# Kernel tuning notes

Measured on AMD Instinct MI355X. Metric: run time of the kernel, lower is better.

The kernel has to match this reference:

```python
import jax, jax.numpy as jnp
import numpy as np

B, T, H, V = 2, 1024, 4096, 32000
IGNORE_INDEX = -100
BETA = 0.1


def setup_inputs() -> dict:
    key = jax.random.key(0)
    k = jax.random.split(key, 6)
    scale = 1.0 / np.sqrt(H)  # Linear default init scale
    return {
        "x": jax.random.normal(k[0], (B, T, H), jnp.float32),
        "ref_x": jax.random.normal(k[1], (B, T, H), jnp.float32),
        "y": jax.random.randint(k[2], (B, T), 0, V),
        "preference_labels": jax.random.randint(k[3], (B,), 0, 2).astype(bool),
        "W": jax.random.normal(k[4], (V, H), jnp.float32) * scale,
        "ref_W": jax.random.normal(k[5], (V, H), jnp.float32) * scale,
    }


def _avg_logp(h, W, y):
    # h: (B,T,H), W: (V,H), y: (B,T) -> per-sequence average target log-prob (B,)
    logits = jnp.einsum("bth,vh->btv", h, W)
    logp = jax.nn.log_softmax(logits, axis=-1)
    tok_logp = jnp.take_along_axis(logp, jnp.clip(y, 0, V - 1)[..., None], axis=-1)[..., 0]
    mask = (y != IGNORE_INDEX).astype(tok_logp.dtype)
    # average_log_prob=True: mean over non-ignored tokens
    return jnp.sum(tok_logp * mask, axis=-1) / jnp.maximum(jnp.sum(mask, axis=-1), 1.0)


def reference(x, ref_x, y, preference_labels, W, ref_W):
    policy_logps = _avg_logp(x, W, y)            # (B,)
    ref_logps = _avg_logp(ref_x, ref_W, y)       # (B,), no-grad path in original
    logratios = policy_logps - ref_logps
    multiplier = jnp.where(preference_labels, 1.0, -1.0)
    # KTO loss with kl=None: 1 - sigmoid(beta * logratios * multiplier)
    losses = 1.0 - jax.nn.sigmoid(BETA * logratios * multiplier)
    return jnp.sum(losses) / y.shape[0]
```

## Files before the change

### kernel.cpp

```cpp
#include <hip/hip_runtime.h>
#include <hip/hip_bf16.h>
#include <math.h>

#define TT 1024
#define MM 2048
#define HH 4096
#define VV 32000
#define BETA_ 0.1f
#define NPB (VV/64)

#define BM 256
#define BN 256
#define BK 64
#define NT (HH/BK)

typedef short short8 __attribute__((ext_vector_type(8)));
typedef float f32x4 __attribute__((ext_vector_type(4)));

__device__ inline unsigned f2bf1(float f) {
    union { float f; unsigned u; } v; v.f = f;
    return (v.u + 0x7fffu + ((v.u >> 16) & 1u)) >> 16;
}
__device__ inline uint2 pack4(float4 a) {
    uint2 r;
    r.x = f2bf1(a.x) | (f2bf1(a.y) << 16);
    r.y = f2bf1(a.z) | (f2bf1(a.w) << 16);
    return r;
}

__device__ __forceinline__ void gload_lds16(const void* g, void* l) {
    __builtin_amdgcn_global_load_lds(
        (const __attribute__((address_space(1))) void*)(uintptr_t)g,
        (__attribute__((address_space(3))) void*)(unsigned)(uintptr_t)l,
        16, 0, 0);
}

__global__ __launch_bounds__(256) void conv_bf16(
    const float* __restrict__ src, unsigned short* __restrict__ dst, int n8)
{
    int i = blockIdx.x * 256 + threadIdx.x;
    const int stride = gridDim.x * 256;
    for (; i < n8; i += stride) {
        const float4* s = (const float4*)src + 2 * (size_t)i;
        float4 a = s[0], b = s[1];
        uint2 lo = pack4(a), hi = pack4(b);
        *(uint4*)(dst + (size_t)i * 8) = make_uint4(lo.x, lo.y, hi.x, hi.y);
    }
}

__global__ __launch_bounds__(512, 2) void kto_logits_lse_bf16_8p(
    const unsigned short* __restrict__ Xb, const unsigned short* __restrict__ Wb,
    float2* __restrict__ part)
{
    __shared__ __align__(16) unsigned char lds[131072];

    const int tid  = threadIdx.x;
    const int lane = tid & 63;
    const int wave = tid >> 6;
    const int wr   = wave >> 2;
    const int wc   = wave & 3;
    const int lrow = lane & 15;
    const int lgrp = lane >> 4;

    const int fid  = blockIdx.y * gridDim.x + blockIdx.x;
    const int swz  = (fid & 7) * 125 + (fid >> 3);
    const int tile_m = (swz & 7) * BM;
    const int tile_n = (swz >> 3) * BN;

    const int scol = ((lane & 7) * 8) ^ ((lane >> 3) << 3);

    f32x4 acc[8][4];
#pragma unroll
    for (int i = 0; i < 8; ++i)
#pragma unroll
        for (int j = 0; j < 4; ++j) acc[i][j] = f32x4{0.f, 0.f, 0.f, 0.f};

#define STAGE_HALF(S)                                                         \
    do { int s_ = (S);                                                        \
        if (s_ < 4 * NT) {                                                    \
            int ts_ = s_ >> 2, kind_ = s_ & 3, buf_ = ts_ & 1;                \
            int isA_ = kind_ >> 1, half_ = kind_ & 1;                         \
            const unsigned short* base_ = isA_                                \
                ? Xb + (size_t)tile_m * HH : Wb + (size_t)tile_n * HH;        \
            unsigned char* lb_ = lds + (isA_ ? 0 : 65536) + buf_ * 32768;     \
            _Pragma("unroll")                                                 \
            for (int c_ = 0; c_ < 2; ++c_) {                                  \
                int rt_ = half_ * 128 + wave * 16 + c_ * 8;                   \
                gload_lds16(base_ + (size_t)(rt_ + (lane >> 3)) * HH          \
                                  + ts_ * 64 + scol,                          \
                            lb_ + rt_ * 128);                                 \
            }                                                                 \
        } } while (0)

#define LOAD_A(DST, MH)                                                       \
    _Pragma("unroll") for (int m_ = 0; m_ < 4; ++m_)                          \
    _Pragma("unroll") for (int kk_ = 0; kk_ < 2; ++kk_) {                     \
        int rr_ = wr * 128 + (MH) * 64 + m_ * 16 + lrow;                      \
        DST[m_][kk_] = *(const short8*)(ldsAp + rr_ * 128 +                   \
            ((kk_ * 64 + lgrp * 16) ^ ((rr_ & 7) << 4))); }

#define LOAD_B(DST, NH)                                                       \
    _Pragma("unroll") for (int n_ = 0; n_ < 2; ++n_)                          \
    _Pragma("unroll") for (int kk_ = 0; kk_ < 2; ++kk_) {                     \
        int rb_ = wc * 64 + (NH) * 32 + n_ * 16 + lrow;                       \
        DST[n_][kk_] = *(const short8*)(ldsBp + rb_ * 128 +                   \
            ((kk_ * 64 + lgrp * 16) ^ ((rb_ & 7) << 4))); }

#define MFMA16(AF, BF, MB, NB)                                                \
    __builtin_amdgcn_s_setprio(1);                                            \
    _Pragma("unroll") for (int m_ = 0; m_ < 4; ++m_)                          \
    _Pragma("unroll") for (int n_ = 0; n_ < 2; ++n_)                          \
    _Pragma("unroll") for (int kk_ = 0; kk_ < 2; ++kk_)                       \
        acc[(MB) + m_][(NB) + n_] = __builtin_amdgcn_mfma_f32_16x16x32_bf16(  \
            AF[m_][kk_], BF[n_][kk_], acc[(MB) + m_][(NB) + n_], 0, 0, 0);    \
    __builtin_amdgcn_s_setprio(0);

#define SBAR()                                                                \
    __builtin_amdgcn_sched_barrier(0);                                        \
    __builtin_amdgcn_s_barrier();                                             \
    __builtin_amdgcn_sched_barrier(0);

#pragma unroll
    for (int s = 0; s < 6; ++s) STAGE_HALF(s);

    for (int t = 0; t < NT; ++t) {
        const int p = t & 1;
        const unsigned char* ldsAp = lds + p * 32768;
        const unsigned char* ldsBp = lds + 65536 + p * 32768;
        short8 afa[4][2], afb[4][2], bfa[2][2], bfb[2][2];

        STAGE_HALF(4 * t + 6);
        if (t < NT - 1) { asm volatile("s_waitcnt vmcnt(6)" ::: "memory"); }
        else            { asm volatile("s_waitcnt vmcnt(0)" ::: "memory"); }
        SBAR();
        LOAD_A(afa, 0);
        LOAD_B(bfa, 0);
        MFMA16(afa, bfa, 0, 0);
        SBAR();
        STAGE_HALF(4 * t + 7);
        LOAD_B(bfb, 1);
        MFMA16(afa, bfb, 0, 2);
        SBAR();
        STAGE_HALF(4 * t + 8);
        LOAD_A(afb, 1);
        MFMA16(afb, bfa, 4, 0);
        SBAR();
        STAGE_HALF(4 * t + 9);
        MFMA16(afb, bfb, 4, 2);
        SBAR();
    }

    const int nb = (tile_n >> 6) + wc;
#pragma unroll
    for (int mi = 0; mi < 8; ++mi) {
#pragma unroll
        for (int r = 0; r < 4; ++r) {
            float v0 = acc[mi][0][r], v1 = acc[mi][1][r], v2 = acc[mi][2][r], v3 = acc[mi][3][r];
            float mx = fmaxf(fmaxf(v0, v1), fmaxf(v2, v3));
#pragma unroll
            for (int d = 1; d < 16; d <<= 1) mx = fmaxf(mx, __shfl_xor(mx, d, 64));
            float s = __expf(v0 - mx) + __expf(v1 - mx) + __expf(v2 - mx) + __expf(v3 - mx);
#pragma unroll
            for (int d = 1; d < 16; d <<= 1) s += __shfl_xor(s, d, 64);
            if (lrow == 0) {
                int rowg = tile_m + wr * 128 + mi * 16 + lgrp * 4 + r;
                part[(size_t)rowg * NPB + nb] = make_float2(mx, s);
            }
        }
    }
}

__global__ __launch_bounds__(256) void kto_logits_lse(
    const float* __restrict__ X, const float* __restrict__ Wt,
    float2* __restrict__ part)
{
    __shared__ __align__(16) unsigned char ldsf[(128 + 128) * BK * 2];
    unsigned char* ldsA = ldsf;
    unsigned char* ldsB = ldsf + 128 * BK * 2;

    const int tid    = threadIdx.x;
    const int tile_m = blockIdx.x * 128;
    const int tile_n = blockIdx.y * 128;
    const int srow   = tid >> 1;
    const int shalf  = tid & 1;
    const int lane   = tid & 63;
    const int wave   = tid >> 6;
    const int wm     = (wave >> 1) * 64;
    const int wn     = (wave & 1) * 64;
    const int lrow   = lane & 15;
    const int lgrp   = lane >> 4;

    f32x4 acc[4][4];
#pragma unroll
    for (int i = 0; i < 4; ++i)
#pragma unroll
        for (int j = 0; j < 4; ++j) acc[i][j] = f32x4{0.f, 0.f, 0.f, 0.f};

    const float4* gA = (const float4*)(X  + (size_t)(tile_m + srow) * HH) + shalf * 8;
    const float4* gB = (const float4*)(Wt + (size_t)(tile_n + srow) * HH) + shalf * 8;
    const int swzf = (srow & 7) << 4;

    for (int k0 = 0; k0 < HH; k0 += BK) {
        float4 a[8], b[8];
#pragma unroll
        for (int j = 0; j < 8; ++j) a[j] = gA[j];
#pragma unroll
        for (int j = 0; j < 8; ++j) b[j] = gB[j];
        gA += BK / 4; gB += BK / 4;

        __syncthreads();
#pragma unroll
        for (int j = 0; j < 4; ++j) {
            uint2 lo = pack4(a[2*j]), hi = pack4(a[2*j+1]);
            uint4 qa = make_uint4(lo.x, lo.y, hi.x, hi.y);
            lo = pack4(b[2*j]); hi = pack4(b[2*j+1]);
            uint4 qb = make_uint4(lo.x, lo.y, hi.x, hi.y);
            int kb = shalf * 64 + 16 * j;
            *(uint4*)(ldsA + srow * 128 + (kb ^ swzf)) = qa;
            *(uint4*)(ldsB + srow * 128 + (kb ^ swzf)) = qb;
        }
        __syncthreads();

#pragma unroll
        for (int kk = 0; kk < 2; ++kk) {
            short8 af[4], bf[4];
#pragma unroll
            for (int mi = 0; mi < 4; ++mi) {
                int r = wm + mi * 16 + lrow;
                af[mi] = *(const short8*)(ldsA + r * 128 + ((kk * 64 + lgrp * 16) ^ ((r & 7) << 4)));
            }
#pragma unroll
            for (int ni = 0; ni < 4; ++ni) {
                int r = wn + ni * 16 + lrow;
                bf[ni] = *(const short8*)(ldsB + r * 128 + ((kk * 64 + lgrp * 16) ^ ((r & 7) << 4)));
            }
#pragma unroll
            for (int mi = 0; mi < 4; ++mi)
#pragma unroll
                for (int ni = 0; ni < 4; ++ni)
                    acc[mi][ni] = __builtin_amdgcn_mfma_f32_16x16x32_bf16(af[mi], bf[ni], acc[mi][ni], 0, 0, 0);
        }
    }

    const int nb = blockIdx.y * 2 + (wave & 1);
#pragma unroll
    for (int mi = 0; mi < 4; ++mi) {
#pragma unroll
        for (int r = 0; r < 4; ++r) {
            float v0 = acc[mi][0][r], v1 = acc[mi][1][r], v2 = acc[mi][2][r], v3 = acc[mi][3][r];
            float mx = fmaxf(fmaxf(v0, v1), fmaxf(v2, v3));
#pragma unroll
            for (int d = 1; d < 16; d <<= 1) mx = fmaxf(mx, __shfl_xor(mx, d, 64));
            float s = __expf(v0 - mx) + __expf(v1 - mx) + __expf(v2 - mx) + __expf(v3 - mx);
#pragma unroll
            for (int d = 1; d < 16; d <<= 1) s += __shfl_xor(s, d, 64);
            if (lrow == 0) {
                int rowg = tile_m + wm + mi * 16 + lgrp * 4 + r;
                part[(size_t)rowg * NPB + nb] = make_float2(mx, s);
            }
        }
    }
}

__global__ __launch_bounds__(256) void kto_target(
    const float* __restrict__ X, const float* __restrict__ RX,
    const float* __restrict__ W, const float* __restrict__ RW,
    const int* __restrict__ Y,
    float* __restrict__ tgtP, float* __restrict__ tgtR)
{
    __shared__ float red[2][4];
    const int t = blockIdx.x;
    int yt = Y[t]; yt = yt < 0 ? 0 : (yt > VV - 1 ? VV - 1 : yt);
    const float4* x4  = (const float4*)(X  + (size_t)t  * HH);
    const float4* rx4 = (const float4*)(RX + (size_t)t  * HH);
    const float4* w4  = (const float4*)(W  + (size_t)yt * HH);
    const float4* rw4 = (const float4*)(RW + (size_t)yt * HH);
    float sp = 0.f, sr = 0.f;
    for (int i = threadIdx.x; i < HH / 4; i += 256) {
        float4 a = x4[i],  w = w4[i];
        sp += a.x * w.x + a.y * w.y + a.z * w.z + a.w * w.w;
        float4 bq = rx4[i], rw = rw4[i];
        sr += bq.x * rw.x + bq.y * rw.y + bq.z * rw.z + bq.w * rw.w;
    }
#pragma unroll
    for (int d = 1; d < 64; d <<= 1) { sp += __shfl_xor(sp, d, 64); sr += __shfl_xor(sr, d, 64); }
    int wv = threadIdx.x >> 6, ln = threadIdx.x & 63;
    if (ln == 0) { red[0][wv] = sp; red[1][wv] = sr; }
    __syncthreads();
    if (threadIdx.x == 0) {
        tgtP[t] = red[0][0] + red[0][1] + red[0][2] + red[0][3];
        tgtR[t] = red[1][0] + red[1][1] + red[1][2] + red[1][3];
    }
}

__device__ inline float2 mrg(float2 a, float2 b) {
    if (b.x == -INFINITY) return a;
    if (a.x == -INFINITY) return b;
    if (a.x >= b.x) { a.y += b.y * __expf(b.x - a.x); return a; }
    b.y += a.y * __expf(a.x - b.x); return b;
}

__global__ __launch_bounds__(256) void kto_lse_combine(
    const float2* __restrict__ partP, const float2* __restrict__ partR,
    const float* __restrict__ tgtP, const float* __restrict__ tgtR,
    float* __restrict__ tokP, float* __restrict__ tokR)
{
    __shared__ float2 redP[4], redR[4];
    const int t = blockIdx.x;
    float2 ap = make_float2(-INFINITY, 0.f), ar = ap;
    for (int i = threadIdx.x; i < NPB; i += 256) {
        ap = mrg(ap, partP[(size_t)t * NPB + i]);
        ar = mrg(ar, partR[(size_t)t * NPB + i]);
    }
#pragma unroll
    for (int d = 1; d < 64; d <<= 1) {
        float2 o;
        o.x = __shfl_xor(ap.x, d, 64); o.y = __shfl_xor(ap.y, d, 64); ap = mrg(ap, o);
        o.x = __shfl_xor(ar.x, d, 64); o.y = __shfl_xor(ar.y, d, 64); ar = mrg(ar, o);
    }
    int wv = threadIdx.x >> 6, ln = threadIdx.x & 63;
    if (ln == 0) { redP[wv] = ap; redR[wv] = ar; }
    __syncthreads();
    if (threadIdx.x == 0) {
        float2 p = mrg(mrg(redP[0], redP[1]), mrg(redP[2], redP[3]));
        float2 r = mrg(mrg(redR[0], redR[1]), mrg(redR[2], redR[3]));
        tokP[t] = tgtP[t] - (p.x + logf(p.y));
        tokR[t] = tgtR[t] - (r.x + logf(r.y));
    }
}

__global__ __launch_bounds__(1024) void kto_final(
    const float* __restrict__ tokP, const float* __restrict__ tokR,
    const int* __restrict__ Y, const unsigned char* __restrict__ pref,
    float* __restrict__ out)
{
    __shared__ float red[6][16];
    const int t = threadIdx.x;
    float m0 = (Y[t]      != -100) ? 1.f : 0.f;
    float m1 = (Y[TT + t] != -100) ? 1.f : 0.f;
    float v[6];
    v[0] = m0 * tokP[t];       v[1] = m0 * tokR[t];       v[2] = m0;
    v[3] = m1 * tokP[TT + t];  v[4] = m1 * tokR[TT + t];  v[5] = m1;
#pragma unroll
    for (int d = 1; d < 64; d <<= 1)
#pragma unroll
        for (int j = 0; j < 6; ++j) v[j] += __shfl_xor(v[j], d, 64);
    int wv = threadIdx.x >> 6, ln = threadIdx.x & 63;
    if (ln == 0)
#pragma unroll
        for (int j = 0; j < 6; ++j) red[j][wv] = v[j];
    __syncthreads();
    if (t == 0) {
        float s[6];
#pragma unroll
        for (int j = 0; j < 6; ++j) { s[j] = 0.f; for (int w = 0; w < 16; ++w) s[j] += red[j][w]; }
        bool byteStorage = ((pref[1] | pref[2] | pref[3]) != 0) || (pref[4] > 1) ||
                           ((pref[5] | pref[6] | pref[7]) != 0);
        int l0, l1;
        if (byteStorage) { l0 = pref[0]; l1 = pref[1]; }
        else { l0 = ((const int*)pref)[0]; l1 = ((const int*)pref)[1]; }
        float pl0 = s[0] / fmaxf(s[2], 1.f);
        float rl0 = s[1] / fmaxf(s[2], 1.f);
        float pl1 = s[3] / fmaxf(s[5], 1.f);
        float rl1 = s[4] / fmaxf(s[5], 1.f);
        float lr0 = pl0 - rl0, lr1 = pl1 - rl1;
        float mu0 = l0 ? 1.f : -1.f;
        float mu1 = l1 ? 1.f : -1.f;
        float loss0 = 1.f - 1.f / (1.f + expf(-BETA_ * lr0 * mu0));
        float loss1 = 1.f - 1.f / (1.f + expf(-BETA_ * lr1 * mu1));
        out[0] = 0.5f * (loss0 + loss1);
    }
}

extern "C" void kernel_launch(void* const* d_in, const int* in_sizes, int n_in,
                              void* d_out, int out_size, void* d_ws, size_t ws_size,
                              hipStream_t stream) {
    const float* X  = (const float*)d_in[0];
    const float* RX = (const float*)d_in[1];
    const int*   Y  = (const int*)d_in[2];
    const unsigned char* PL = (const unsigned char*)d_in[3];
    const float* W  = (const float*)d_in[4];
    const float* RW = (const float*)d_in[5];
    float* out = (float*)d_out;

    char* p = (char*)d_ws;
    float2* partP = (float2*)p;                 p += (size_t)MM * NPB * sizeof(float2);
    float2* partR = (float2*)p;                 p += (size_t)MM * NPB * sizeof(float2);
    float*  tgtP  = (float*)p;                  p += MM * sizeof(float);
    float*  tgtR  = (float*)p;                  p += MM * sizeof(float);
    float*  tokP  = (float*)p;                  p += MM * sizeof(float);
    float*  tokR  = (float*)p;                  p += MM * sizeof(float);
    unsigned short* Xbf  = (unsigned short*)p;  p += (size_t)MM * HH * 2;
    unsigned short* RXbf = (unsigned short*)p;  p += (size_t)MM * HH * 2;
    unsigned short* Wbf  = (unsigned short*)p;  p += (size_t)VV * HH * 2;
    const size_t need = (size_t)(p - (char*)d_ws);

    if (ws_size >= need) {
        dim3 ggrid(MM / BM, VV / BN);
        conv_bf16<<<512,  256, 0, stream>>>(X,  Xbf,  (int)((size_t)MM * HH / 8));
        conv_bf16<<<512,  256, 0, stream>>>(RX, RXbf, (int)((size_t)MM * HH / 8));
        conv_bf16<<<2048, 256, 0, stream>>>(W,  Wbf,  (int)((size_t)VV * HH / 8));
        kto_logits_lse_bf16_8p<<<ggrid, 512, 0, stream>>>(Xbf, Wbf, partP);
        conv_bf16<<<2048, 256, 0, stream>>>(RW, Wbf,  (int)((size_t)VV * HH / 8));
        kto_logits_lse_bf16_8p<<<ggrid, 512, 0, stream>>>(RXbf, Wbf, partR);
    } else {
        dim3 fgrid(MM / 128, VV / 128);
        kto_logits_lse<<<fgrid, 256, 0, stream>>>(X,  W,  partP);
        kto_logits_lse<<<fgrid, 256, 0, stream>>>(RX, RW, partR);
    }
    kto_target<<<MM, 256, 0, stream>>>(X, RX, W, RW, Y, tgtP, tgtR);
    kto_lse_combine<<<MM, 256, 0, stream>>>(partP, partR, tgtP, tgtR, tokP, tokR);
    kto_final<<<1, 1024, 0, stream>>>(tokP, tokR, Y, PL, out);
}
```

Before: 1.213 ms.

## Fuse fp32-to-bf16 weight conversion into the GEMM B-tile load path

```diff
diff --git a/kernel.cpp b/kernel.cpp
--- a/kernel.cpp
+++ b/kernel.cpp
@@ -48,8 +48,8 @@
     }
 }
 
-__global__ __launch_bounds__(512, 2) void kto_logits_lse_bf16_8p(
-    const unsigned short* __restrict__ Xb, const unsigned short* __restrict__ Wb,
+__global__ __launch_bounds__(512, 2) void kto_logits_lse_v7(
+    const unsigned short* __restrict__ Xb, const float* __restrict__ Wf,
     float2* __restrict__ part)
 {
     __shared__ __align__(16) unsigned char lds[131072];
@@ -75,20 +75,52 @@
 #pragma unroll
         for (int j = 0; j < 4; ++j) acc[i][j] = f32x4{0.f, 0.f, 0.f, 0.f};
 
-#define STAGE_HALF(S)                                                         \
-    do { int s_ = (S);                                                        \
-        if (s_ < 4 * NT) {                                                    \
-            int ts_ = s_ >> 2, kind_ = s_ & 3, buf_ = ts_ & 1;                \
-            int isA_ = kind_ >> 1, half_ = kind_ & 1;                         \
-            const unsigned short* base_ = isA_                                \
-                ? Xb + (size_t)tile_m * HH : Wb + (size_t)tile_n * HH;        \
-            unsigned char* lb_ = lds + (isA_ ? 0 : 65536) + buf_ * 32768;     \
+    float4 breg[8];
+
+#define STAGE_A(T)                                                            \
+    do { int ta_ = (T);                                                       \
+        if (ta_ < NT) {                                                       \
+            unsigned char* la_ = lds + (ta_ & 1) * 32768;                     \
+            _Pragma("unroll")                                                 \
+            for (int h_ = 0; h_ < 2; ++h_)                                    \
             _Pragma("unroll")                                                 \
             for (int c_ = 0; c_ < 2; ++c_) {                                  \
-                int rt_ = half_ * 128 + wave * 16 + c_ * 8;                   \
-                gload_lds16(base_ + (size_t)(rt_ + (lane >> 3)) * HH          \
-                                  + ts_ * 64 + scol,                          \
-                            lb_ + rt_ * 128);                                 \
+                int rt_ = h_ * 128 + wave * 16 + c_ * 8;                      \
+                gload_lds16(Xb + (size_t)(tile_m + rt_ + (lane >> 3)) * HH    \
+                               + ta_ * 64 + scol,                             \
+                            la_ + rt_ * 128);                                 \
+            }                                                                 \
+        } } while (0)
+
+#define ISSUE_B(T)                                                            \
+    do { int tb_ = (T);                                                       \
+        if (tb_ < NT) {                                                       \
+            _Pragma("unroll")                                                 \
+            for (int h_ = 0; h_ < 2; ++h_) {                                  \
+                int rt_ = h_ * 128 + wave * 16 + (lane >> 2);                 \
+                const float4* src_ = (const float4*)(Wf +                     \
+                    (size_t)(tile_n + rt_) * HH + tb_ * 64 + (lane & 3) * 16);\
+                _Pragma("unroll")                                             \
+                for (int j_ = 0; j_ < 4; ++j_)                                \
+                    breg[h_ * 4 + j_] = src_[j_];                             \
+            }                                                                 \
+        } } while (0)
+
+#define PACK_WRITE_B(T)                                                       \
+    do { int tb_ = (T);                                                       \
+        if (tb_ < NT) {                                                       \
+            unsigned char* lb_ = lds + 65536 + (tb_ & 1) * 32768;             \
+            _Pragma("unroll")                                                 \
+            for (int h_ = 0; h_ < 2; ++h_) {                                  \
+                int rt_ = h_ * 128 + wave * 16 + (lane >> 2);                 \
+                _Pragma("unroll")                                             \
+                for (int jj_ = 0; jj_ < 2; ++jj_) {                           \
+                    uint2 lo_ = pack4(breg[h_ * 4 + jj_ * 2]);                \
+                    uint2 hi_ = pack4(breg[h_ * 4 + jj_ * 2 + 1]);            \
+                    *(uint4*)(lb_ + rt_ * 128 +                               \
+                        (((lane & 3) * 32 + jj_ * 16) ^ ((rt_ & 7) << 4))) =  \
+                        make_uint4(lo_.x, lo_.y, hi_.x, hi_.y);               \
+                }                                                             \
             }                                                                 \
         } } while (0)
 
@@ -107,21 +139,25 @@
             ((kk_ * 64 + lgrp * 16) ^ ((rb_ & 7) << 4))); }
 
 #define MFMA16(AF, BF, MB, NB)                                                \
-    __builtin_amdgcn_s_setprio(1);                                            \
     _Pragma("unroll") for (int m_ = 0; m_ < 4; ++m_)                          \
     _Pragma("unroll") for (int n_ = 0; n_ < 2; ++n_)                          \
     _Pragma("unroll") for (int kk_ = 0; kk_ < 2; ++kk_)                       \
         acc[(MB) + m_][(NB) + n_] = __builtin_amdgcn_mfma_f32_16x16x32_bf16(  \
-            AF[m_][kk_], BF[n_][kk_], acc[(MB) + m_][(NB) + n_], 0, 0, 0);    \
-    __builtin_amdgcn_s_setprio(0);
+            AF[m_][kk_], BF[n_][kk_], acc[(MB) + m_][(NB) + n_], 0, 0, 0);
 
 #define SBAR()                                                                \
     __builtin_amdgcn_sched_barrier(0);                                        \
     __builtin_amdgcn_s_barrier();                                             \
     __builtin_amdgcn_sched_barrier(0);
 
-#pragma unroll
-    for (int s = 0; s < 6; ++s) STAGE_HALF(s);
+    ISSUE_B(0);
+    STAGE_A(0);
+    asm volatile("s_waitcnt vmcnt(4)" ::: "memory");
+    PACK_WRITE_B(0);
+    ISSUE_B(1);
+    asm volatile("s_waitcnt vmcnt(8)" ::: "memory");
+    asm volatile("s_waitcnt lgkmcnt(0)" ::: "memory");
+    SBAR();
 
     for (int t = 0; t < NT; ++t) {
         const int p = t & 1;
@@ -129,24 +165,26 @@
         const unsigned char* ldsBp = lds + 65536 + p * 32768;
         short8 afa[4][2], afb[4][2], bfa[2][2], bfb[2][2];
 
-        STAGE_HALF(4 * t + 6);
-        if (t < NT - 1) { asm volatile("s_waitcnt vmcnt(6)" ::: "memory"); }
-        else            { asm volatile("s_waitcnt vmcnt(0)" ::: "memory"); }
-        SBAR();
         LOAD_A(afa, 0);
         LOAD_B(bfa, 0);
+        LOAD_B(bfb, 1);
+        STAGE_A(t + 1);
+        __builtin_amdgcn_s_setprio(1);
         MFMA16(afa, bfa, 0, 0);
+        MFMA16(afa, bfb, 0, 2);
+        __builtin_amdgcn_s_setprio(0);
         SBAR();
-        STAGE_HALF(4 * t + 7);
-        LOAD_B(bfb, 1);
-        MFMA16(afa, bfb, 0, 2);
-        SBAR();
-        STAGE_HALF(4 * t + 8);
         LOAD_A(afb, 1);
+        asm volatile("s_waitcnt vmcnt(4)" ::: "memory");
+        PACK_WRITE_B(t + 1);
+        ISSUE_B(t + 2);
+        __builtin_amdgcn_s_setprio(1);
         MFMA16(afb, bfa, 4, 0);
-        SBAR();
-        STAGE_HALF(4 * t + 9);
         MFMA16(afb, bfb, 4, 2);
+        __builtin_amdgcn_s_setprio(0);
+        if (t < NT - 2) { asm volatile("s_waitcnt vmcnt(8)" ::: "memory"); }
+        else            { asm volatile("s_waitcnt vmcnt(0)" ::: "memory"); }
+        asm volatile("s_waitcnt lgkmcnt(0)" ::: "memory");
         SBAR();
     }
 
@@ -242,7 +280,7 @@
         }
     }
 
-    const int nb = blockIdx.y * 2 + (wave & 1);
+    const int nbf = blockIdx.y * 2 + (wave & 1);
 #pragma unroll
     for (int mi = 0; mi < 4; ++mi) {
 #pragma unroll
@@ -256,7 +294,7 @@
             for (int d = 1; d < 16; d <<= 1) s += __shfl_xor(s, d, 64);
             if (lrow == 0) {
                 int rowg = tile_m + wm + mi * 16 + lgrp * 4 + r;
-                part[(size_t)rowg * NPB + nb] = make_float2(mx, s);
+                part[(size_t)rowg * NPB + nbf] = make_float2(mx, s);
             }
         }
     }
@@ -392,17 +430,14 @@
     float*  tokR  = (float*)p;                  p += MM * sizeof(float);
     unsigned short* Xbf  = (unsigned short*)p;  p += (size_t)MM * HH * 2;
     unsigned short* RXbf = (unsigned short*)p;  p += (size_t)MM * HH * 2;
-    unsigned short* Wbf  = (unsigned short*)p;  p += (size_t)VV * HH * 2;
     const size_t need = (size_t)(p - (char*)d_ws);
 
     if (ws_size >= need) {
         dim3 ggrid(MM / BM, VV / BN);
-        conv_bf16<<<512,  256, 0, stream>>>(X,  Xbf,  (int)((size_t)MM * HH / 8));
-        conv_bf16<<<512,  256, 0, stream>>>(RX, RXbf, (int)((size_t)MM * HH / 8));
-        conv_bf16<<<2048, 256, 0, stream>>>(W,  Wbf,  (int)((size_t)VV * HH / 8));
-        kto_logits_lse_bf16_8p<<<ggrid, 512, 0, stream>>>(Xbf, Wbf, partP);
-        conv_bf16<<<2048, 256, 0, stream>>>(RW, Wbf,  (int)((size_t)VV * HH / 8));
-        kto_logits_lse_bf16_8p<<<ggrid, 512, 0, stream>>>(RXbf, Wbf, partR);
+        conv_bf16<<<512, 256, 0, stream>>>(X,  Xbf,  (int)((size_t)MM * HH / 8));
+        conv_bf16<<<512, 256, 0, stream>>>(RX, RXbf, (int)((size_t)MM * HH / 8));
+        kto_logits_lse_v7<<<ggrid, 512, 0, stream>>>(Xbf,  W,  partP);
+        kto_logits_lse_v7<<<ggrid, 512, 0, stream>>>(RXbf, RW, partR);
     } else {
         dim3 fgrid(MM / 128, VV / 128);
         kto_logits_lse<<<fgrid, 256, 0, stream>>>(X,  W,  partP);
```

After: 1.272 ms. +4.9%, slower.

## Fuse ref_W bf16 conversion into policy GEMM and restructure K-loop barriers

Applied to the files above, without the earlier changes.

```diff
diff --git a/kernel.cpp b/kernel.cpp
--- a/kernel.cpp
+++ b/kernel.cpp
@@ -26,6 +26,11 @@
     r.x = f2bf1(a.x) | (f2bf1(a.y) << 16);
     r.y = f2bf1(a.z) | (f2bf1(a.w) << 16);
     return r;
+}
+__device__ inline unsigned cvtpk(float lo, float hi) {
+    union { __hip_bfloat162 h; unsigned u; } v;
+    v.h = __float22bfloat162_rn(make_float2(lo, hi));
+    return v.u;
 }
 
 __device__ __forceinline__ void gload_lds16(const void* g, void* l) {
@@ -48,9 +53,11 @@
     }
 }
 
-__global__ __launch_bounds__(512, 2) void kto_logits_lse_bf16_8p(
+template<bool CONV>
+__global__ __launch_bounds__(512, 2) void kto_logits_lse_v9(
     const unsigned short* __restrict__ Xb, const unsigned short* __restrict__ Wb,
-    float2* __restrict__ part)
+    float2* __restrict__ part,
+    const float* __restrict__ csrc, unsigned short* __restrict__ cdst)
 {
     __shared__ __align__(16) unsigned char lds[131072];
 
@@ -107,13 +114,11 @@
             ((kk_ * 64 + lgrp * 16) ^ ((rb_ & 7) << 4))); }
 
 #define MFMA16(AF, BF, MB, NB)                                                \
-    __builtin_amdgcn_s_setprio(1);                                            \
     _Pragma("unroll") for (int m_ = 0; m_ < 4; ++m_)                          \
     _Pragma("unroll") for (int n_ = 0; n_ < 2; ++n_)                          \
     _Pragma("unroll") for (int kk_ = 0; kk_ < 2; ++kk_)                       \
         acc[(MB) + m_][(NB) + n_] = __builtin_amdgcn_mfma_f32_16x16x32_bf16(  \
-            AF[m_][kk_], BF[n_][kk_], acc[(MB) + m_][(NB) + n_], 0, 0, 0);    \
-    __builtin_amdgcn_s_setprio(0);
+            AF[m_][kk_], BF[n_][kk_], acc[(MB) + m_][(NB) + n_], 0, 0, 0);
 
 #define SBAR()                                                                \
     __builtin_amdgcn_sched_barrier(0);                                        \
@@ -122,31 +127,43 @@
 
 #pragma unroll
     for (int s = 0; s < 6; ++s) STAGE_HALF(s);
+    asm volatile("s_waitcnt vmcnt(4)" ::: "memory");
+    SBAR();
 
     for (int t = 0; t < NT; ++t) {
         const int p = t & 1;
         const unsigned char* ldsAp = lds + p * 32768;
         const unsigned char* ldsBp = lds + 65536 + p * 32768;
         short8 afa[4][2], afb[4][2], bfa[2][2], bfb[2][2];
-
+        float4 cv;
+
+        if (CONV)
+            cv = *(const float4*)(csrc + ((size_t)fid * NT + t) * 2048 + tid * 4);
         STAGE_HALF(4 * t + 6);
-        if (t < NT - 1) { asm volatile("s_waitcnt vmcnt(6)" ::: "memory"); }
-        else            { asm volatile("s_waitcnt vmcnt(0)" ::: "memory"); }
-        SBAR();
+        STAGE_HALF(4 * t + 7);
         LOAD_A(afa, 0);
         LOAD_B(bfa, 0);
+        LOAD_B(bfb, 1);
+        __builtin_amdgcn_s_setprio(1);
         MFMA16(afa, bfa, 0, 0);
+        MFMA16(afa, bfb, 0, 2);
+        __builtin_amdgcn_s_setprio(0);
         SBAR();
-        STAGE_HALF(4 * t + 7);
-        LOAD_B(bfb, 1);
-        MFMA16(afa, bfb, 0, 2);
-        SBAR();
+        if (CONV) {
+            uint2 q = make_uint2(cvtpk(cv.x, cv.y), cvtpk(cv.z, cv.w));
+            *(uint2*)(cdst + ((size_t)fid * NT + t) * 2048 + tid * 4) = q;
+        }
         STAGE_HALF(4 * t + 8);
+        STAGE_HALF(4 * t + 9);
         LOAD_A(afb, 1);
+        __builtin_amdgcn_s_setprio(1);
         MFMA16(afb, bfa, 4, 0);
-        SBAR();
-        STAGE_HALF(4 * t + 9);
         MFMA16(afb, bfb, 4, 2);
+        __builtin_amdgcn_s_setprio(0);
+        if (t < NT - 2) {
+            if (CONV) { asm volatile("s_waitcnt vmcnt(5)" ::: "memory"); }
+            else      { asm volatile("s_waitcnt vmcnt(4)" ::: "memory"); }
+        } else        { asm volatile("s_waitcnt vmcnt(0)" ::: "memory"); }
         SBAR();
     }
 
@@ -242,7 +259,7 @@
         }
     }
 
-    const int nb = blockIdx.y * 2 + (wave & 1);
+    const int nbf = blockIdx.y * 2 + (wave & 1);
 #pragma unroll
     for (int mi = 0; mi < 4; ++mi) {
 #pragma unroll
@@ -256,7 +273,7 @@
             for (int d = 1; d < 16; d <<= 1) s += __shfl_xor(s, d, 64);
             if (lrow == 0) {
                 int rowg = tile_m + wm + mi * 16 + lgrp * 4 + r;
-                part[(size_t)rowg * NPB + nb] = make_float2(mx, s);
+                part[(size_t)rowg * NPB + nbf] = make_float2(mx, s);
             }
         }
     }
@@ -393,16 +410,25 @@
     unsigned short* Xbf  = (unsigned short*)p;  p += (size_t)MM * HH * 2;
     unsigned short* RXbf = (unsigned short*)p;  p += (size_t)MM * HH * 2;
     unsigned short* Wbf  = (unsigned short*)p;  p += (size_t)VV * HH * 2;
-    const size_t need = (size_t)(p - (char*)d_ws);
-
-    if (ws_size >= need) {
-        dim3 ggrid(MM / BM, VV / BN);
+    const size_t need1 = (size_t)(p - (char*)d_ws);
+    unsigned short* RWbf = (unsigned short*)p;  p += (size_t)VV * HH * 2;
+    const size_t need2 = (size_t)(p - (char*)d_ws);
+
+    dim3 ggrid(MM / BM, VV / BN);
+
+    if (ws_size >= need2) {
         conv_bf16<<<512,  256, 0, stream>>>(X,  Xbf,  (int)((size_t)MM * HH / 8));
         conv_bf16<<<512,  256, 0, stream>>>(RX, RXbf, (int)((size_t)MM * HH / 8));
         conv_bf16<<<2048, 256, 0, stream>>>(W,  Wbf,  (int)((size_t)VV * HH / 8));
-        kto_logits_lse_bf16_8p<<<ggrid, 512, 0, stream>>>(Xbf, Wbf, partP);
+        kto_logits_lse_v9<true ><<<ggrid, 512, 0, stream>>>(Xbf,  Wbf,  partP, RW, RWbf);
+        kto_logits_lse_v9<false><<<ggrid, 512, 0, stream>>>(RXbf, RWbf, partR, nullptr, nullptr);
+    } else if (ws_size >= need1) {
+        conv_bf16<<<512,  256, 0, stream>>>(X,  Xbf,  (int)((size_t)MM * HH / 8));
+        conv_bf16<<<512,  256, 0, stream>>>(RX, RXbf, (int)((size_t)MM * HH / 8));
+        conv_bf16<<<2048, 256, 0, stream>>>(W,  Wbf,  (int)((size_t)VV * HH / 8));
+        kto_logits_lse_v9<false><<<ggrid, 512, 0, stream>>>(Xbf, Wbf, partP, nullptr, nullptr);
         conv_bf16<<<2048, 256, 0, stream>>>(RW, Wbf,  (int)((size_t)VV * HH / 8));
-        kto_logits_lse_bf16_8p<<<ggrid, 512, 0, stream>>>(RXbf, Wbf, partR);
+        kto_logits_lse_v9<false><<<ggrid, 512, 0, stream>>>(RXbf, Wbf, partR, nullptr, nullptr);
     } else {
         dim3 fgrid(MM / 128, VV / 128);
         kto_logits_lse<<<fgrid, 256, 0, stream>>>(X,  W,  partP);
```

Result: no change. 1.235 ms (+1.8%).
